# Optimization experiments

Hardware: AMD Instinct MI355X
Metric: run time of the kernel (lower is better)

Reference implementation:

```python
import jax, jax.numpy as jnp
import numpy as np

HIDDEN = 2048
N_HEADS = 16
N_KV = 4
HEAD_DIM = 128
EPS = 1e-6
B, S = 2, 2048


def rms_norm(x, w, eps=EPS):
    xf = x.astype(jnp.float32)
    var = jnp.mean(xf * xf, axis=-1, keepdims=True)
    return (w * (xf * jax.lax.rsqrt(var + eps))).astype(x.dtype)


def rotate_half(x):
    half = x.shape[-1] // 2
    return jnp.concatenate([-x[..., half:], x[..., :half]], axis=-1)


def setup_inputs() -> dict:
    key = jax.random.key(0)
    ks = jax.random.split(key, 9)
    inv_freq = 1.0 / (10000.0 ** (np.arange(0, HEAD_DIM, 2) / HEAD_DIM))
    ang = np.arange(S)[:, None] * inv_freq[None, :]
    ang = np.concatenate([ang, ang], axis=-1)  # [S, HEAD_DIM]
    return {
        "hidden_states": jax.random.normal(ks[0], (B, S, HIDDEN), jnp.float32),
        "cos": jnp.asarray(np.cos(ang), jnp.float32),
        "sin": jnp.asarray(np.sin(ang), jnp.float32),
        "Wq": jax.random.normal(ks[1], (HIDDEN, N_HEADS * HEAD_DIM), jnp.float32) * 0.02,
        "Wk": jax.random.normal(ks[2], (HIDDEN, N_KV * HEAD_DIM), jnp.float32) * 0.02,
        "Wv": jax.random.normal(ks[3], (HIDDEN, N_KV * HEAD_DIM), jnp.float32) * 0.02,
        "Wo": jax.random.normal(ks[4], (N_HEADS * HEAD_DIM, HIDDEN), jnp.float32) * 0.02,
        "q_norm_w": jnp.ones((HEAD_DIM,), jnp.float32),
        "k_norm_w": jnp.ones((HEAD_DIM,), jnp.float32),
    }


def reference(hidden_states, cos, sin, Wq, Wk, Wv, Wo, q_norm_w, k_norm_w):
    b, s, _ = hidden_states.shape
    n_rep = N_HEADS // N_KV
    scaling = HEAD_DIM ** -0.5

    q = (hidden_states @ Wq).reshape(b, s, N_HEADS, HEAD_DIM)
    k = (hidden_states @ Wk).reshape(b, s, N_KV, HEAD_DIM)
    v = (hidden_states @ Wv).reshape(b, s, N_KV, HEAD_DIM)

    q = rms_norm(q, q_norm_w)
    k = rms_norm(k, k_norm_w)

    q = q.transpose(0, 2, 1, 3)  # [b, h, s, d]
    k = k.transpose(0, 2, 1, 3)  # [b, kv, s, d]
    v = v.transpose(0, 2, 1, 3)

    c = cos[None, None]  # [1,1,s,d]
    si = sin[None, None]
    q = q * c + rotate_half(q) * si
    k = k * c + rotate_half(k) * si

    # repeat kv heads to match query heads
    k = jnp.repeat(k, n_rep, axis=1)
    v = jnp.repeat(v, n_rep, axis=1)

    scores = jnp.einsum("bhqd,bhkd->bhqk", q, k) * scaling
    causal = jnp.triu(jnp.full((s, s), -jnp.inf, jnp.float32), k=1)
    scores = scores + causal
    attn = jax.nn.softmax(scores.astype(jnp.float32), axis=-1).astype(q.dtype)

    out = jnp.einsum("bhqk,bhkd->bhqd", attn, v)
    out = out.transpose(0, 2, 1, 3).reshape(b, s, N_HEADS * HEAD_DIM)
    return out @ Wo
```

## Files before the change

kernel.cpp:

```cpp
#include <hip/hip_runtime.h>

typedef float floatx4 __attribute__((ext_vector_type(4)));
typedef short short8 __attribute__((ext_vector_type(8)));

#define HIDDEN 2048
#define NH 16
#define NKV 4
#define HD 128
#define NB 2
#define SEQ 2048
#define MT (NB * SEQ)
#define NQKV 3072

__device__ __forceinline__ unsigned short f2bf(float x) {
  union { float f; unsigned u; } v; v.f = x;
  unsigned r = v.u + 0x7FFFu + ((v.u >> 16) & 1u);
  return (unsigned short)(r >> 16);
}

__global__ void cast_bf16_kernel(const float* __restrict__ in,
                                 unsigned short* __restrict__ out, int n4) {
  int i = blockIdx.x * 256 + threadIdx.x;
  if (i >= n4) return;
  float4 v = ((const float4*)in)[i];
  ushort4 o;
  o.x = f2bf(v.x); o.y = f2bf(v.y); o.z = f2bf(v.z); o.w = f2bf(v.w);
  ((ushort4*)out)[i] = o;
}

__global__ void wtrans_kernel(const float* __restrict__ Wq,
                              const float* __restrict__ Wk,
                              const float* __restrict__ Wv,
                              const float* __restrict__ Wo,
                              unsigned short* __restrict__ wqkvt,
                              unsigned short* __restrict__ wot) {
  __shared__ float tile[32][33];
  int z = blockIdx.z;
  int nt = blockIdx.x * 32;
  int k0 = blockIdx.y * 32;
  const float* src;
  unsigned short* dst;
  int Nd, scol0, drow0;
  if (z == 0) {
    src = Wq; Nd = 2048; scol0 = nt; drow0 = nt; dst = wqkvt;
  } else if (z == 1) {
    src = Wo; Nd = 2048; scol0 = nt; drow0 = nt; dst = wot;
  } else {
    if (nt >= 1024) return;
    Nd = 512; dst = wqkvt; drow0 = 2048 + nt;
    if (nt < 512) { src = Wk; scol0 = nt; }
    else          { src = Wv; scol0 = nt - 512; }
  }
  int tx = threadIdx.x, ty = threadIdx.y;
  for (int i = 0; i < 32; i += 8)
    tile[ty + i][tx] = src[(size_t)(k0 + ty + i) * Nd + scol0 + tx];
  __syncthreads();
  for (int i = 0; i < 32; i += 8)
    dst[(size_t)(drow0 + ty + i) * HIDDEN + k0 + tx] = f2bf(tile[tx][ty + i]);
}

__global__ __launch_bounds__(256, 3)
void gemm_bf16_kernel(const unsigned short* __restrict__ A,
                      const unsigned short* __restrict__ Bt,
                      float* __restrict__ C, int M, int N, int K) {
  __shared__ unsigned short As[128 * 32];
  __shared__ unsigned short Bs[128 * 32];
  const int tid = threadIdx.x;
  const int wave = tid >> 6, lane = tid & 63;
  const int quad = lane >> 4, l16 = lane & 15;
  const int m0 = blockIdx.x * 128, n0 = blockIdx.y * 128;
  const int wm = (wave >> 1) * 64, wn = (wave & 1) * 64;
  const int srow = lane >> 2;
  const int scol = (lane & 3) * 8;

  floatx4 acc[4][4] = {};

  for (int kt = 0; kt < K; kt += 32) {
    __syncthreads();
#pragma unroll
    for (int t = 0; t < 2; ++t) {
      int q = wave * 2 + t;
      int row = q * 16 + srow;
      __builtin_amdgcn_global_load_lds(
          (const __attribute__((address_space(1))) unsigned int*)&A[(size_t)(m0 + row) * K + kt + scol],
          (__attribute__((address_space(3))) unsigned int*)&As[q * 16 * 32],
          16, 0, 0);
      __builtin_amdgcn_global_load_lds(
          (const __attribute__((address_space(1))) unsigned int*)&Bt[(size_t)(n0 + row) * K + kt + scol],
          (__attribute__((address_space(3))) unsigned int*)&Bs[q * 16 * 32],
          16, 0, 0);
    }
    __syncthreads();
    short8 af[4], bf[4];
#pragma unroll
    for (int i = 0; i < 4; i++)
      af[i] = *(const short8*)&As[(wm + i * 16 + l16) * 32 + quad * 8];
#pragma unroll
    for (int j = 0; j < 4; j++)
      bf[j] = *(const short8*)&Bs[(wn + j * 16 + l16) * 32 + quad * 8];
#pragma unroll
    for (int i = 0; i < 4; i++)
#pragma unroll
      for (int j = 0; j < 4; j++)
        acc[i][j] = __builtin_amdgcn_mfma_f32_16x16x32_bf16(af[i], bf[j], acc[i][j], 0, 0, 0);
  }
#pragma unroll
  for (int i = 0; i < 4; i++) {
    int row = m0 + wm + i * 16 + quad * 4;
#pragma unroll
    for (int j = 0; j < 4; j++) {
      int col = n0 + wn + j * 16 + l16;
#pragma unroll
      for (int r = 0; r < 4; r++)
        C[(size_t)(row + r) * N + col] = acc[i][j][r];
    }
  }
}

__global__ void norm_rope_kernel(const float* __restrict__ X,
                                 const float* __restrict__ qw,
                                 const float* __restrict__ kw,
                                 const float* __restrict__ cosb,
                                 const float* __restrict__ sinb,
                                 unsigned short* __restrict__ Qb,
                                 unsigned short* __restrict__ Kbb)
{
  int rid = blockIdx.x * 4 + (threadIdx.x >> 6);
  int lane = threadIdx.x & 63;
  int m = rid / 20, hh = rid - m * 20;
  int b = m / SEQ, s = m - b * SEQ;
  const float* w;
  const float* x;
  unsigned short* op;
  if (hh < NH) {
    x = X + (size_t)m * NQKV + hh * HD;
    w = qw;
    op = Qb + (size_t)((b * NH + hh) * SEQ + s) * HD;
  } else {
    int hk = hh - NH;
    x = X + (size_t)m * NQKV + 2048 + hk * HD;
    w = kw;
    op = Kbb + (size_t)((b * NKV + hk) * SEQ + s) * HD;
  }
  float x0 = x[lane], x1 = x[lane + 64];
  float ssq = x0 * x0 + x1 * x1;
#pragma unroll
  for (int off = 32; off >= 1; off >>= 1) ssq += __shfl_xor(ssq, off, 64);
  float rr = rsqrtf(ssq * (1.0f / 128.0f) + 1e-6f);
  float xn0 = x0 * rr * w[lane];
  float xn1 = x1 * rr * w[lane + 64];
  float c0 = cosb[s * HD + lane], c1 = cosb[s * HD + lane + 64];
  float s0 = sinb[s * HD + lane], s1 = sinb[s * HD + lane + 64];
  op[lane] = f2bf(xn0 * c0 - xn1 * s0);
  op[lane + 64] = f2bf(xn1 * c1 + xn0 * s1);
}

__global__ void v_transpose_kernel(const float* __restrict__ X,
                                   unsigned short* __restrict__ Vt) {
  __shared__ float tile[32][33];
  int d0 = blockIdx.x * 32;
  int s0 = blockIdx.y * 32;
  int bkv = blockIdx.z;
  int b = bkv >> 2, kv = bkv & 3;
  int tx = threadIdx.x, ty = threadIdx.y;
  const float* src = X + (size_t)(b * SEQ + s0) * NQKV + 2560 + kv * HD + d0;
  for (int i = 0; i < 32; i += 8)
    tile[ty + i][tx] = src[(size_t)(ty + i) * NQKV + tx];
  __syncthreads();
  unsigned short* dst = Vt + (size_t)(bkv * HD + d0) * SEQ + s0;
  for (int i = 0; i < 32; i += 8)
    dst[(size_t)(ty + i) * SEQ + tx] = f2bf(tile[tx][ty + i]);
}

#define LQ 136

__global__ __launch_bounds__(256, 2)
void attn_kernel(const unsigned short* __restrict__ Q,
                 const unsigned short* __restrict__ Kb,
                 const unsigned short* __restrict__ Vt,
                 unsigned short* __restrict__ O) {
  __shared__ unsigned short Qs[64 * LQ];
  __shared__ unsigned short KVs[128 * LQ];
  __shared__ unsigned short Ps[64 * LQ];
  const int tid = threadIdx.x;
  const int wave = tid >> 6, lane = tid & 63;
  const int quad = lane >> 4, l16 = lane & 15;
  const int qt = (SEQ / 64 - 1) - (blockIdx.x >> 5);
  const int bh = blockIdx.x & 31;
  const int b = bh >> 4, h = bh & 15, kvh = h >> 2;
  const int q0 = qt * 64;
  const int nkt = (qt >> 1) + 1;

  const unsigned short* Qg = Q + (size_t)((b * NH + h) * SEQ + q0) * HD;
  for (int c = tid; c < 1024; c += 256) {
    int r = c >> 4, c8 = c & 15;
    *(uint4*)&Qs[r * LQ + c8 * 8] = *(const uint4*)&Qg[r * HD + c8 * 8];
  }

  floatx4 oacc[8] = {};
  float mrow[4] = {-1e30f, -1e30f, -1e30f, -1e30f};
  float lrow[4] = {0.f, 0.f, 0.f, 0.f};
  const float scale = 0.08838834764831845f;
  const unsigned short* Kg0 = Kb + (size_t)((b * NKV + kvh) * SEQ) * HD;
  const unsigned short* Vg0 = Vt + (size_t)((b * NKV + kvh) * HD) * SEQ;

  for (int kt = 0; kt < nkt; ++kt) {
    __syncthreads();
    for (int c = tid; c < 2048; c += 256) {
      int r = c >> 4, c8 = c & 15;
      *(uint4*)&KVs[r * LQ + c8 * 8] = *(const uint4*)&Kg0[(size_t)(kt * 128 + r) * HD + c8 * 8];
    }
    __syncthreads();
    floatx4 sc[8] = {};
#pragma unroll
    for (int ks = 0; ks < 4; ++ks) {
      short8 af = *(const short8*)&Qs[(wave * 16 + l16) * LQ + ks * 32 + quad * 8];
#pragma unroll
      for (int j = 0; j < 8; ++j) {
        short8 bf = *(const short8*)&KVs[(j * 16 + l16) * LQ + ks * 32 + quad * 8];
        sc[j] = __builtin_amdgcn_mfma_f32_16x16x32_bf16(af, bf, sc[j], 0, 0, 0);
      }
    }
#pragma unroll
    for (int j = 0; j < 8; ++j)
#pragma unroll
      for (int r = 0; r < 4; ++r) sc[j][r] *= scale;
    if (kt == nkt - 1) {
      int rowg = q0 + wave * 16 + quad * 4;
#pragma unroll
      for (int j = 0; j < 8; ++j) {
        int col = kt * 128 + j * 16 + l16;
#pragma unroll
        for (int r = 0; r < 4; ++r)
          if (col > rowg + r) sc[j][r] = -1e30f;
      }
    }
    float alpha[4];
#pragma unroll
    for (int r = 0; r < 4; ++r) {
      float mx = sc[0][r];
#pragma unroll
      for (int j = 1; j < 8; ++j) mx = fmaxf(mx, sc[j][r]);
#pragma unroll
      for (int off = 1; off < 16; off <<= 1) mx = fmaxf(mx, __shfl_xor(mx, off, 64));
      float mn = fmaxf(mrow[r], mx);
      alpha[r] = __expf(mrow[r] - mn);
      mrow[r] = mn;
      float rs = 0.f;
#pragma unroll
      for (int j = 0; j < 8; ++j) {
        float p = __expf(sc[j][r] - mn);
        sc[j][r] = p;
        rs += p;
      }
#pragma unroll
      for (int off = 1; off < 16; off <<= 1) rs += __shfl_xor(rs, off, 64);
      lrow[r] = lrow[r] * alpha[r] + rs;
    }
#pragma unroll
    for (int t = 0; t < 8; ++t)
#pragma unroll
      for (int r = 0; r < 4; ++r) oacc[t][r] *= alpha[r];
#pragma unroll
    for (int j = 0; j < 8; ++j)
#pragma unroll
      for (int r = 0; r < 4; ++r)
        Ps[(wave * 16 + quad * 4 + r) * LQ + j * 16 + l16] = f2bf(sc[j][r]);
    __syncthreads();
    for (int c = tid; c < 2048; c += 256) {
      int d = c >> 4, c8 = c & 15;
      *(uint4*)&KVs[d * LQ + c8 * 8] = *(const uint4*)&Vg0[(size_t)d * SEQ + kt * 128 + c8 * 8];
    }
    __syncthreads();
#pragma unroll
    for (int ks = 0; ks < 4; ++ks) {
      short8 af = *(const short8*)&Ps[(wave * 16 + l16) * LQ + ks * 32 + quad * 8];
#pragma unroll
      for (int t = 0; t < 8; ++t) {
        short8 bf = *(const short8*)&KVs[(t * 16 + l16) * LQ + ks * 32 + quad * 8];
        oacc[t] = __builtin_amdgcn_mfma_f32_16x16x32_bf16(af, bf, oacc[t], 0, 0, 0);
      }
    }
  }
  float inv[4];
#pragma unroll
  for (int r = 0; r < 4; ++r) inv[r] = 1.0f / lrow[r];
#pragma unroll
  for (int t = 0; t < 8; ++t) {
    int col = h * HD + t * 16 + l16;
#pragma unroll
    for (int r = 0; r < 4; ++r) {
      int row = q0 + wave * 16 + quad * 4 + r;
      O[(size_t)(b * SEQ + row) * (NH * HD) + col] = f2bf(oacc[t][r] * inv[r]);
    }
  }
}

extern "C" void kernel_launch(void* const* d_in, const int* in_sizes, int n_in,
                              void* d_out, int out_size, void* d_ws, size_t ws_size,
                              hipStream_t stream) {
  const float* hidden = (const float*)d_in[0];
  const float* cosb   = (const float*)d_in[1];
  const float* sinb   = (const float*)d_in[2];
  const float* Wq     = (const float*)d_in[3];
  const float* Wk     = (const float*)d_in[4];
  const float* Wv     = (const float*)d_in[5];
  const float* Wo     = (const float*)d_in[6];
  const float* qw     = (const float*)d_in[7];
  const float* kw     = (const float*)d_in[8];
  (void)in_sizes; (void)n_in; (void)out_size; (void)ws_size;

  char* ws = (char*)d_ws;
  size_t off = 0;
  auto alloc = [&](size_t n) { char* p = ws + off; off += (n + 255) & ~(size_t)255; return p; };

  unsigned short* hb    = (unsigned short*)alloc((size_t)MT * HIDDEN * 2);
  unsigned short* wqkvt = (unsigned short*)alloc((size_t)NQKV * HIDDEN * 2);
  unsigned short* wot   = (unsigned short*)alloc((size_t)2048 * 2048 * 2);
  float* qkvraw = (float*)alloc((size_t)MT * NQKV * 4);
  unsigned short* Qb  = (unsigned short*)alloc((size_t)MT * 2048 * 2);
  unsigned short* Kbb = (unsigned short*)alloc((size_t)MT * 512 * 2);
  unsigned short* Vtb = (unsigned short*)alloc((size_t)MT * 512 * 2);
  unsigned short* Ob  = (unsigned short*)alloc((size_t)MT * 2048 * 2);

  cast_bf16_kernel<<<(MT * HIDDEN / 4) / 256, 256, 0, stream>>>(hidden, hb, MT * HIDDEN / 4);
  dim3 tb(32, 8);
  wtrans_kernel<<<dim3(64, 64, 3), tb, 0, stream>>>(Wq, Wk, Wv, Wo, wqkvt, wot);

  gemm_bf16_kernel<<<dim3(MT / 128, NQKV / 128), 256, 0, stream>>>(hb, wqkvt, qkvraw, MT, NQKV, HIDDEN);

  norm_rope_kernel<<<MT * (NH + NKV) / 4, 256, 0, stream>>>(qkvraw, qw, kw, cosb, sinb, Qb, Kbb);
  v_transpose_kernel<<<dim3(HD / 32, SEQ / 32, NB * NKV), tb, 0, stream>>>(qkvraw, Vtb);

  attn_kernel<<<(SEQ / 64) * 32, 256, 0, stream>>>(Qb, Kbb, Vtb, Ob);

  gemm_bf16_kernel<<<dim3(MT / 128, 16), 256, 0, stream>>>(Ob, wot, (float*)d_out, MT, 2048, 2048);
}
```

Before: 359.9 us.

## Fuse RMSNorm, RoPE and V transpose into QKV GEMM epilogue; keep Q in registers

The QKV projection GEMM now does the per-head RMSNorm and RoPE in its epilogue and writes bf16 Q/K and transposed V directly. This removes the fp32 qkvraw intermediate, its write and re-read, and two separate kernel launches. The epilogue exchanges the partner half of each head and the partial sums of squares through shared memory, which adds barriers and LDS use. Separately, the attention kernel holds its Q fragments in registers instead of LDS and raises the occupancy hint to 3 blocks per SM, at the cost of higher register pressure.

After: 345.8 us. 3.9% less time.

```diff
diff --git a/kernel.cpp b/kernel.cpp
--- a/kernel.cpp
+++ b/kernel.cpp
@@ -117,69 +117,140 @@
   }
 }
 
-__global__ void norm_rope_kernel(const float* __restrict__ X,
-                                 const float* __restrict__ qw,
-                                 const float* __restrict__ kw,
-                                 const float* __restrict__ cosb,
-                                 const float* __restrict__ sinb,
-                                 unsigned short* __restrict__ Qb,
-                                 unsigned short* __restrict__ Kbb)
-{
-  int rid = blockIdx.x * 4 + (threadIdx.x >> 6);
-  int lane = threadIdx.x & 63;
-  int m = rid / 20, hh = rid - m * 20;
-  int b = m / SEQ, s = m - b * SEQ;
-  const float* w;
-  const float* x;
-  unsigned short* op;
-  if (hh < NH) {
-    x = X + (size_t)m * NQKV + hh * HD;
-    w = qw;
-    op = Qb + (size_t)((b * NH + hh) * SEQ + s) * HD;
-  } else {
-    int hk = hh - NH;
-    x = X + (size_t)m * NQKV + 2048 + hk * HD;
-    w = kw;
-    op = Kbb + (size_t)((b * NKV + hk) * SEQ + s) * HD;
-  }
-  float x0 = x[lane], x1 = x[lane + 64];
-  float ssq = x0 * x0 + x1 * x1;
-#pragma unroll
-  for (int off = 32; off >= 1; off >>= 1) ssq += __shfl_xor(ssq, off, 64);
-  float rr = rsqrtf(ssq * (1.0f / 128.0f) + 1e-6f);
-  float xn0 = x0 * rr * w[lane];
-  float xn1 = x1 * rr * w[lane + 64];
-  float c0 = cosb[s * HD + lane], c1 = cosb[s * HD + lane + 64];
-  float s0 = sinb[s * HD + lane], s1 = sinb[s * HD + lane + 64];
-  op[lane] = f2bf(xn0 * c0 - xn1 * s0);
-  op[lane + 64] = f2bf(xn1 * c1 + xn0 * s1);
-}
-
-__global__ void v_transpose_kernel(const float* __restrict__ X,
-                                   unsigned short* __restrict__ Vt) {
-  __shared__ float tile[32][33];
-  int d0 = blockIdx.x * 32;
-  int s0 = blockIdx.y * 32;
-  int bkv = blockIdx.z;
-  int b = bkv >> 2, kv = bkv & 3;
-  int tx = threadIdx.x, ty = threadIdx.y;
-  const float* src = X + (size_t)(b * SEQ + s0) * NQKV + 2560 + kv * HD + d0;
-  for (int i = 0; i < 32; i += 8)
-    tile[ty + i][tx] = src[(size_t)(ty + i) * NQKV + tx];
-  __syncthreads();
-  unsigned short* dst = Vt + (size_t)(bkv * HD + d0) * SEQ + s0;
-  for (int i = 0; i < 32; i += 8)
-    dst[(size_t)(ty + i) * SEQ + tx] = f2bf(tile[tx][ty + i]);
+__global__ __launch_bounds__(256, 3)
+void gemm_qkv_kernel(const unsigned short* __restrict__ A,
+                     const unsigned short* __restrict__ Bt,
+                     const float* __restrict__ qw,
+                     const float* __restrict__ kw,
+                     const float* __restrict__ cosb,
+                     const float* __restrict__ sinb,
+                     unsigned short* __restrict__ Qb,
+                     unsigned short* __restrict__ Kbb,
+                     unsigned short* __restrict__ Vt) {
+  __shared__ __align__(16) unsigned short As[128 * 32];
+  __shared__ __align__(16) unsigned short Bs[128 * 32];
+  __shared__ __align__(16) float pscr[4 * 64 * 20];
+  __shared__ float pssq[2][128];
+  const int tid = threadIdx.x;
+  const int wave = tid >> 6, lane = tid & 63;
+  const int quad = lane >> 4, l16 = lane & 15;
+  const int m0 = blockIdx.x * 128, n0 = blockIdx.y * 128;
+  const int wm = (wave >> 1) * 64, wn = (wave & 1) * 64;
+  const int srow = lane >> 2;
+  const int scol = (lane & 3) * 8;
+
+  floatx4 acc[4][4] = {};
+
+  for (int kt = 0; kt < HIDDEN; kt += 32) {
+    __syncthreads();
+#pragma unroll
+    for (int t = 0; t < 2; ++t) {
+      int q = wave * 2 + t;
+      int row = q * 16 + srow;
+      __builtin_amdgcn_global_load_lds(
+          (const __attribute__((address_space(1))) unsigned int*)&A[(size_t)(m0 + row) * HIDDEN + kt + scol],
+          (__attribute__((address_space(3))) unsigned int*)&As[q * 16 * 32],
+          16, 0, 0);
+      __builtin_amdgcn_global_load_lds(
+          (const __attribute__((address_space(1))) unsigned int*)&Bt[(size_t)(n0 + row) * HIDDEN + kt + scol],
+          (__attribute__((address_space(3))) unsigned int*)&Bs[q * 16 * 32],
+          16, 0, 0);
+    }
+    __syncthreads();
+    short8 af[4], bf[4];
+#pragma unroll
+    for (int i = 0; i < 4; i++)
+      af[i] = *(const short8*)&As[(wm + i * 16 + l16) * 32 + quad * 8];
+#pragma unroll
+    for (int j = 0; j < 4; j++)
+      bf[j] = *(const short8*)&Bs[(wn + j * 16 + l16) * 32 + quad * 8];
+#pragma unroll
+    for (int i = 0; i < 4; i++)
+#pragma unroll
+      for (int j = 0; j < 4; j++)
+        acc[i][j] = __builtin_amdgcn_mfma_f32_16x16x32_bf16(af[i], bf[j], acc[i][j], 0, 0, 0);
+  }
+
+  const int head = n0 >> 7;
+  if (head >= NH + NKV) {
+    const int kv = head - (NH + NKV);
+#pragma unroll
+    for (int i = 0; i < 4; ++i) {
+      int m = m0 + wm + i * 16 + quad * 4;
+      int b = m >> 11, sbase = m & (SEQ - 1);
+#pragma unroll
+      for (int j = 0; j < 4; ++j) {
+        int d = wn + j * 16 + l16;
+        ushort4 pk;
+        pk.x = f2bf(acc[i][j][0]); pk.y = f2bf(acc[i][j][1]);
+        pk.z = f2bf(acc[i][j][2]); pk.w = f2bf(acc[i][j][3]);
+        *(ushort4*)&Vt[((size_t)(b * NKV + kv) * HD + d) * SEQ + sbase] = pk;
+      }
+    }
+    return;
+  }
+
+  const float* w = (head < NH) ? qw : kw;
+  float wown[4], wpar[4];
+#pragma unroll
+  for (int j = 0; j < 4; ++j) {
+    wown[j] = w[wn + j * 16 + l16];
+    wpar[j] = w[(wn ^ 64) + j * 16 + l16];
+  }
+#pragma unroll
+  for (int i = 0; i < 4; ++i) {
+    float sq[4];
+#pragma unroll
+    for (int r = 0; r < 4; ++r) {
+      float s2 = acc[i][0][r] * acc[i][0][r] + acc[i][1][r] * acc[i][1][r] +
+                 acc[i][2][r] * acc[i][2][r] + acc[i][3][r] * acc[i][3][r];
+#pragma unroll
+      for (int off = 1; off < 16; off <<= 1) s2 += __shfl_xor(s2, off, 64);
+      sq[r] = s2;
+    }
+    if (l16 == 0)
+      *(float4*)&pssq[wn >> 6][wm + i * 16 + quad * 4] = make_float4(sq[0], sq[1], sq[2], sq[3]);
+#pragma unroll
+    for (int j = 0; j < 4; ++j)
+      *(float4*)&pscr[(wave * 64 + j * 16 + l16) * 20 + quad * 4] = *(float4*)&acc[i][j];
+    __syncthreads();
+    float4 oss = *(const float4*)&pssq[(wn >> 6) ^ 1][wm + i * 16 + quad * 4];
+    float rr[4];
+    rr[0] = rsqrtf((sq[0] + oss.x) * (1.0f / 128.0f) + 1e-6f);
+    rr[1] = rsqrtf((sq[1] + oss.y) * (1.0f / 128.0f) + 1e-6f);
+    rr[2] = rsqrtf((sq[2] + oss.z) * (1.0f / 128.0f) + 1e-6f);
+    rr[3] = rsqrtf((sq[3] + oss.w) * (1.0f / 128.0f) + 1e-6f);
+    int mbase = m0 + wm + i * 16 + quad * 4;
+    int b = mbase >> 11, sbase = mbase & (SEQ - 1);
+#pragma unroll
+    for (int j = 0; j < 4; ++j) {
+      float4 par = *(const float4*)&pscr[((wave ^ 1) * 64 + j * 16 + l16) * 20 + quad * 4];
+      float pr[4] = {par.x, par.y, par.z, par.w};
+      int d = wn + j * 16 + l16;
+      unsigned short* dst = (head < NH)
+          ? Qb + ((size_t)(b * NH + head) * SEQ + sbase) * HD + d
+          : Kbb + ((size_t)(b * NKV + (head - NH)) * SEQ + sbase) * HD + d;
+#pragma unroll
+      for (int r = 0; r < 4; ++r) {
+        int s = sbase + r;
+        float c = cosb[s * HD + d], sn = sinb[s * HD + d];
+        float xo = acc[i][j][r] * rr[r] * wown[j];
+        float xp = pr[r] * rr[r] * wpar[j];
+        float out = (wn == 0) ? (xo * c - xp * sn) : (xo * c + xp * sn);
+        dst[(size_t)r * HD] = f2bf(out);
+      }
+    }
+    __syncthreads();
+  }
 }
 
 #define LQ 136
 
-__global__ __launch_bounds__(256, 2)
+__global__ __launch_bounds__(256, 3)
 void attn_kernel(const unsigned short* __restrict__ Q,
                  const unsigned short* __restrict__ Kb,
                  const unsigned short* __restrict__ Vt,
                  unsigned short* __restrict__ O) {
-  __shared__ unsigned short Qs[64 * LQ];
   __shared__ unsigned short KVs[128 * LQ];
   __shared__ unsigned short Ps[64 * LQ];
   const int tid = threadIdx.x;
@@ -192,10 +263,10 @@
   const int nkt = (qt >> 1) + 1;
 
   const unsigned short* Qg = Q + (size_t)((b * NH + h) * SEQ + q0) * HD;
-  for (int c = tid; c < 1024; c += 256) {
-    int r = c >> 4, c8 = c & 15;
-    *(uint4*)&Qs[r * LQ + c8 * 8] = *(const uint4*)&Qg[r * HD + c8 * 8];
-  }
+  short8 qf[4];
+#pragma unroll
+  for (int ks = 0; ks < 4; ++ks)
+    qf[ks] = *(const short8*)&Qg[(size_t)(wave * 16 + l16) * HD + ks * 32 + quad * 8];
 
   floatx4 oacc[8] = {};
   float mrow[4] = {-1e30f, -1e30f, -1e30f, -1e30f};
@@ -214,11 +285,10 @@
     floatx4 sc[8] = {};
 #pragma unroll
     for (int ks = 0; ks < 4; ++ks) {
-      short8 af = *(const short8*)&Qs[(wave * 16 + l16) * LQ + ks * 32 + quad * 8];
 #pragma unroll
       for (int j = 0; j < 8; ++j) {
         short8 bf = *(const short8*)&KVs[(j * 16 + l16) * LQ + ks * 32 + quad * 8];
-        sc[j] = __builtin_amdgcn_mfma_f32_16x16x32_bf16(af, bf, sc[j], 0, 0, 0);
+        sc[j] = __builtin_amdgcn_mfma_f32_16x16x32_bf16(qf[ks], bf, sc[j], 0, 0, 0);
       }
     }
 #pragma unroll
@@ -317,7 +387,6 @@
   unsigned short* hb    = (unsigned short*)alloc((size_t)MT * HIDDEN * 2);
   unsigned short* wqkvt = (unsigned short*)alloc((size_t)NQKV * HIDDEN * 2);
   unsigned short* wot   = (unsigned short*)alloc((size_t)2048 * 2048 * 2);
-  float* qkvraw = (float*)alloc((size_t)MT * NQKV * 4);
   unsigned short* Qb  = (unsigned short*)alloc((size_t)MT * 2048 * 2);
   unsigned short* Kbb = (unsigned short*)alloc((size_t)MT * 512 * 2);
   unsigned short* Vtb = (unsigned short*)alloc((size_t)MT * 512 * 2);
@@ -327,10 +396,8 @@
   dim3 tb(32, 8);
   wtrans_kernel<<<dim3(64, 64, 3), tb, 0, stream>>>(Wq, Wk, Wv, Wo, wqkvt, wot);
 
-  gemm_bf16_kernel<<<dim3(MT / 128, NQKV / 128), 256, 0, stream>>>(hb, wqkvt, qkvraw, MT, NQKV, HIDDEN);
-
-  norm_rope_kernel<<<MT * (NH + NKV) / 4, 256, 0, stream>>>(qkvraw, qw, kw, cosb, sinb, Qb, Kbb);
-  v_transpose_kernel<<<dim3(HD / 32, SEQ / 32, NB * NKV), tb, 0, stream>>>(qkvraw, Vtb);
+  gemm_qkv_kernel<<<dim3(MT / 128, NQKV / 128), 256, 0, stream>>>(
+      hb, wqkvt, qw, kw, cosb, sinb, Qb, Kbb, Vtb);
 
   attn_kernel<<<(SEQ / 64) * 32, 256, 0, stream>>>(Qb, Kbb, Vtb, Ob);
 
```
